# Performance work log

Hardware: AMD Instinct MI355X
Metric: run time of the kernel (lower is better)

The kernel has to match this reference:

```python
import jax, jax.numpy as jnp
import numpy as np

N = 50000       # nodes
E = 800000      # edges
D_IN = 128      # input_dim
HID = 256       # hidden_dim
HEADS = 4
FH = HID // 4   # per-head out dim = 64
OUT = 8         # output_dim
NEG_SLOPE = 0.2 # GATConv leaky_relu slope


def setup_inputs() -> dict:
    key = jax.random.key(0)
    ks = jax.random.split(key, 16)
    def glorot(k, shape):
        fan_in, fan_out = shape[0], shape[-1]
        s = jnp.sqrt(6.0 / (fan_in + fan_out))
        return jax.random.uniform(k, shape, jnp.float32, -s, s)
    inp = {
        "x": jax.random.normal(ks[0], (N, D_IN), jnp.float32),
        "edge_index": jax.random.randint(ks[1], (2, E), 0, N, jnp.int64),
        # GCN layers
        "W1": glorot(ks[2], (D_IN, HID)), "b1": jnp.zeros((HID,), jnp.float32),
        "W2": glorot(ks[3], (HID, HID)), "b2": jnp.zeros((HID,), jnp.float32),
        "W3": glorot(ks[4], (HID, HID // 2)), "b3": jnp.zeros((HID // 2,), jnp.float32),
        # GAT layer: in = HID//2 = 128, out per head = FH, 4 heads concat -> HID
        "Wg": glorot(ks[5], (HID // 2, HEADS * FH)),
        "a_src": glorot(ks[6], (HEADS, FH)),
        "a_dst": glorot(ks[7], (HEADS, FH)),
        "bg": jnp.zeros((HEADS * FH,), jnp.float32),
        # classifier MLP: HID -> HID//2 -> HID//4 -> OUT
        "Wc1": glorot(ks[8], (HID, HID // 2)), "bc1": jnp.zeros((HID // 2,), jnp.float32),
        "Wc2": glorot(ks[9], (HID // 2, HID // 4)), "bc2": jnp.zeros((HID // 4,), jnp.float32),
        "Wc3": glorot(ks[10], (HID // 4, OUT)), "bc3": jnp.zeros((OUT,), jnp.float32),
    }
    return inp


def _with_self_loops(edge_index, n):
    loop = jnp.arange(n, dtype=edge_index.dtype)
    src = jnp.concatenate([edge_index[0], loop])
    dst = jnp.concatenate([edge_index[1], loop])
    return src, dst


def gcn_conv(x, W, b, src, dst, n):
    # PyG GCNConv: h = X W; out = D^{-1/2}(A+I)D^{-1/2} h + b (self loops in src/dst)
    h = x @ W
    deg = jax.ops.segment_sum(jnp.ones_like(dst, jnp.float32), dst, num_segments=n)
    dinv = jnp.where(deg > 0, jax.lax.rsqrt(deg), 0.0)
    norm = dinv[src] * dinv[dst]                      # [E+N]
    out = jax.ops.segment_sum(h[src] * norm[:, None], dst, num_segments=n)
    return out + b


def gat_conv(x, Wg, a_src, a_dst, bg, src, dst, n):
    # PyG GATConv (eval mode, no attn dropout), self loops included in src/dst
    h = (x @ Wg).reshape(n, HEADS, FH)                # [N,H,F]
    al_s = jnp.einsum('nhf,hf->nh', h, a_src)         # [N,H]
    al_d = jnp.einsum('nhf,hf->nh', h, a_dst)
    e = jax.nn.leaky_relu(al_s[src] + al_d[dst], NEG_SLOPE)  # [E+N,H]
    m = jax.ops.segment_max(e, dst, num_segments=n)   # per-dst stable softmax
    ex = jnp.exp(e - m[dst])
    den = jax.ops.segment_sum(ex, dst, num_segments=n)
    alpha = ex / den[dst]                             # [E+N,H]
    out = jax.ops.segment_sum(h[src] * alpha[:, :, None], dst, num_segments=n)
    return out.reshape(n, HEADS * FH) + bg


def reference(x, edge_index, W1, b1, W2, b2, W3, b3, Wg, a_src, a_dst, bg,
              Wc1, bc1, Wc2, bc2, Wc3, bc3):
    n = x.shape[0]
    src, dst = _with_self_loops(edge_index, n)
    h1 = jax.nn.relu(gcn_conv(x, W1, b1, src, dst, n))
    h2 = jax.nn.relu(gcn_conv(h1, W2, b2, src, dst, n)) + h1
    h3 = jax.nn.relu(gcn_conv(h2, W3, b3, src, dst, n))
    h_att = jax.nn.relu(gat_conv(h3, Wg, a_src, a_dst, bg, src, dst, n))
    h_pooled = jnp.mean(h_att, axis=0, keepdims=True)           # [1, HID]
    z = jax.nn.relu(h_pooled @ Wc1 + bc1)
    z = jax.nn.relu(z @ Wc2 + bc2)
    return z @ Wc3 + bc3                                        # [1, OUT]
```

## Files before the change

### kernel.cpp

```cpp
#include <hip/hip_runtime.h>
#include <hip/hip_bf16.h>

#define NNODES 50000
#define NEDGES 800000
#define EN 850000
#define SCAN_B 196

typedef __attribute__((ext_vector_type(8))) short bf16x8;
typedef __attribute__((ext_vector_type(4))) float f32x4;

__device__ __forceinline__ float bf2f(unsigned short u) {
    return __uint_as_float(((unsigned)u) << 16);
}
__device__ __forceinline__ float bflo(unsigned u) { return __uint_as_float(u << 16); }
__device__ __forceinline__ float bfhi(unsigned u) { return __uint_as_float(u & 0xffff0000u); }
__device__ __forceinline__ unsigned short f2bf(float x) {
    unsigned u = __float_as_uint(x);
    u += 0x7fffu + ((u >> 16) & 1u);
    return (unsigned short)(u >> 16);
}
__device__ __forceinline__ unsigned pack2bf(float a, float b) {
    return (unsigned)f2bf(a) | ((unsigned)f2bf(b) << 16);
}
__device__ __forceinline__ void acc8(float* acc, uint4 v, float wg) {
    acc[0] += bflo(v.x) * wg; acc[1] += bfhi(v.x) * wg;
    acc[2] += bflo(v.y) * wg; acc[3] += bfhi(v.y) * wg;
    acc[4] += bflo(v.z) * wg; acc[5] += bfhi(v.z) * wg;
    acc[6] += bflo(v.w) * wg; acc[7] += bfhi(v.w) * wg;
}

__device__ __forceinline__ void split_bf(float x, unsigned short& h, unsigned short& l) {
    unsigned u = __float_as_uint(x);
    h = (unsigned short)(u >> 16);
    float r = x - __uint_as_float(u & 0xffff0000u);
    l = (unsigned short)(__float_as_uint(r) >> 16);
}
__device__ __forceinline__ void do_split(const float* W, unsigned short* Wh, unsigned short* Wl,
                                         int i, int K, int N) {
    int n = i / K, k = i - n * K;
    unsigned short h, l;
    split_bf(W[(size_t)k * N + n], h, l);
    Wh[i] = h; Wl[i] = l;
}

__global__ __launch_bounds__(256) void prep_kernel(const int* __restrict__ ei, float* __restrict__ deg,
                                                   const float* __restrict__ x, unsigned short* __restrict__ xbf,
                                                   const float* __restrict__ W1, const float* __restrict__ W2,
                                                   const float* __restrict__ W3, const float* __restrict__ Wg,
                                                   const float* __restrict__ asr, const float* __restrict__ ads,
                                                   unsigned short* __restrict__ W1th, unsigned short* __restrict__ W1tl,
                                                   unsigned short* __restrict__ W2th, unsigned short* __restrict__ W2tl,
                                                   unsigned short* __restrict__ W3th, unsigned short* __restrict__ W3tl,
                                                   unsigned short* __restrict__ Wgth, unsigned short* __restrict__ Wgtl,
                                                   float* __restrict__ asp, float* __restrict__ adp) {
    int idx = blockIdx.x * 256 + threadIdx.x;
    atomicAdd(&deg[ei[NEDGES + idx]], 1.0f);
    {
        float4 a = *(const float4*)&x[(size_t)idx * 8];
        float4 b = *(const float4*)&x[(size_t)idx * 8 + 4];
        uint4 o;
        o.x = pack2bf(a.x, a.y); o.y = pack2bf(a.z, a.w);
        o.z = pack2bf(b.x, b.y); o.w = pack2bf(b.z, b.w);
        *(uint4*)&xbf[(size_t)idx * 8] = o;
    }
    if (idx < 32768)        do_split(W1, W1th, W1tl, idx, 128, 256);
    else if (idx < 98304)   do_split(W2, W2th, W2tl, idx - 32768, 256, 256);
    else if (idx < 131072)  do_split(W3, W3th, W3tl, idx - 98304, 256, 128);
    else if (idx < 163840)  do_split(Wg, Wgth, Wgtl, idx - 131072, 128, 256);
    else if (idx < 164864) {
        int i0 = idx - 163840;
        int which = i0 >> 9;
        int h = (i0 >> 7) & 3;
        int k = i0 & 127;
        const float* av = (which ? ads : asr) + h * 64;
        const float* wg = Wg + (size_t)k * 256 + h * 64;
        float s = 0.f;
#pragma unroll
        for (int c = 0; c < 64; ++c) s += wg[c] * av[c];
        (which ? adp : asp)[h * 128 + k] = s;
    }
}

__global__ __launch_bounds__(256) void scan_part1(const float* __restrict__ deg, int* __restrict__ row,
                                                  int* __restrict__ bsum, float* __restrict__ dinv) {
    __shared__ int sdata[256];
    int t = threadIdx.x;
    int idx = blockIdx.x * 256 + t;
    float dg = idx < NNODES ? deg[idx] : 0.f;
    if (idx < NNODES) dinv[idx] = rsqrtf(dg + 1.0f);
    int v = idx < NNODES ? (int)dg + 1 : 0;
    sdata[t] = v;
    __syncthreads();
    for (int off = 1; off < 256; off <<= 1) {
        int tmp = t >= off ? sdata[t - off] : 0;
        __syncthreads();
        sdata[t] += tmp;
        __syncthreads();
    }
    if (idx < NNODES) row[idx] = sdata[t] - v;
    if (t == 255) bsum[blockIdx.x] = sdata[255];
}

__global__ __launch_bounds__(256) void scan_part2(int* __restrict__ bsum, int* __restrict__ bofs,
                                                  int* __restrict__ row) {
    __shared__ int sdata[256];
    int t = threadIdx.x;
    int v = t < SCAN_B ? bsum[t] : 0;
    sdata[t] = v;
    __syncthreads();
    for (int off = 1; off < 256; off <<= 1) {
        int tmp = t >= off ? sdata[t - off] : 0;
        __syncthreads();
        sdata[t] += tmp;
        __syncthreads();
    }
    if (t < SCAN_B) bofs[t] = sdata[t] - v;
    if (t == SCAN_B - 1) row[NNODES] = EN - (sdata[t] - v);
}

__global__ __launch_bounds__(256) void scatter_kernel(const int* __restrict__ ei, const int* __restrict__ row,
                                                      const int* __restrict__ bofs,
                                                      int* __restrict__ cursor, const float* __restrict__ dinv,
                                                      uint2* __restrict__ csr) {
    int e = blockIdx.x * blockDim.x + threadIdx.x;
    if (e >= EN) return;
    int s, d;
    if (e < NEDGES) { s = ei[e]; d = ei[NEDGES + e]; } else { s = e - NEDGES; d = s; }
    int pos = row[d] + bofs[d >> 8] + atomicAdd(&cursor[d], 1);
    csr[pos] = make_uint2((unsigned)s, __float_as_uint(dinv[s] * dinv[d]));
}

template<int MODE>
__global__ __launch_bounds__(256) void gemm_bf(const unsigned short* __restrict__ A,
                                               const unsigned short* __restrict__ Wth,
                                               const unsigned short* __restrict__ Wtl,
                                               const float* __restrict__ bias,
                                               unsigned short* __restrict__ C, int M, int K, int Nc) {
    __shared__ unsigned short As[128][40];
    __shared__ unsigned short Bh[128][40], Bl[128][40];
    int t = threadIdx.x;
    int row0 = blockIdx.x * 128, col0 = blockIdx.y * 128;
    int lane = t & 63, w = t >> 6;
    int mb = (w >> 1) * 64, nb = (w & 1) * 64;
    int lr = lane & 15, kg = (lane >> 4) * 8;

    f32x4 acc[4][4];
#pragma unroll
    for (int i = 0; i < 4; ++i)
#pragma unroll
        for (int j = 0; j < 4; ++j) acc[i][j] = (f32x4){0.f, 0.f, 0.f, 0.f};

    for (int k0 = 0; k0 < K; k0 += 32) {
#pragma unroll
        for (int it = 0; it < 2; ++it) {
            int q = it * 256 + t;
            int row = q >> 2, seg = (q & 3) * 8;
            int grow = row0 + row;
            uint4 v = make_uint4(0, 0, 0, 0);
            if (grow < M) v = *(const uint4*)&A[(size_t)grow * K + k0 + seg];
            *(uint4*)&As[row][seg] = v;
        }
#pragma unroll
        for (int it = 0; it < 2; ++it) {
            int o = it * 256 + t;
            int n = o >> 2, ko = (o & 3) * 8;
            size_t g = (size_t)(col0 + n) * K + k0 + ko;
            *(uint4*)&Bh[n][ko] = *(const uint4*)&Wth[g];
            *(uint4*)&Bl[n][ko] = *(const uint4*)&Wtl[g];
        }
        __syncthreads();

        bf16x8 a[4], bh[4], bl[4];
#pragma unroll
        for (int mf = 0; mf < 4; ++mf) a[mf] = *(const bf16x8*)&As[mb + mf * 16 + lr][kg];
#pragma unroll
        for (int nf = 0; nf < 4; ++nf) {
            bh[nf] = *(const bf16x8*)&Bh[nb + nf * 16 + lr][kg];
            bl[nf] = *(const bf16x8*)&Bl[nb + nf * 16 + lr][kg];
        }
#pragma unroll
        for (int mf = 0; mf < 4; ++mf)
#pragma unroll
            for (int nf = 0; nf < 4; ++nf) {
                acc[mf][nf] = __builtin_amdgcn_mfma_f32_16x16x32_bf16(a[mf], bh[nf], acc[mf][nf], 0, 0, 0);
                acc[mf][nf] = __builtin_amdgcn_mfma_f32_16x16x32_bf16(a[mf], bl[nf], acc[mf][nf], 0, 0, 0);
            }
        __syncthreads();
    }

#pragma unroll
    for (int nf = 0; nf < 4; ++nf) {
        int col = col0 + nb + nf * 16 + lr;
        float bv = (MODE == 1) ? bias[col] : 0.f;
#pragma unroll
        for (int mf = 0; mf < 4; ++mf) {
#pragma unroll
            for (int r = 0; r < 4; ++r) {
                int row = row0 + mb + mf * 16 + (lane >> 4) * 4 + r;
                if (row < M) {
                    float v = acc[mf][nf][r];
                    if (MODE == 1) v = fmaxf(v + bv, 0.f);
                    C[(size_t)row * Nc + col] = f2bf(v);
                }
            }
        }
    }
}

template<int NC, int MODE>
__global__ __launch_bounds__(256) void gcn_agg_bf(const unsigned short* __restrict__ h, const int* __restrict__ row,
                                                  const int* __restrict__ bofs, const uint2* __restrict__ csr,
                                                  const float* __restrict__ b, const unsigned short* __restrict__ res,
                                                  const float* __restrict__ asp, const float* __restrict__ adp,
                                                  float* __restrict__ als, float* __restrict__ ald,
                                                  unsigned short* __restrict__ out) {
    int wid = (int)((blockIdx.x * blockDim.x + threadIdx.x) >> 6);
    if (wid >= NNODES) return;
    int lane = threadIdx.x & 63;
    constexpr int LPE = NC / 8;
    constexpr int EPI = 64 / LPE;
    int sub = lane / LPE, li = lane % LPE;
    int col = li * 8;
    float acc[8];
#pragma unroll
    for (int i = 0; i < 8; ++i) acc[i] = 0.f;
    int j0 = row[wid] + bofs[wid >> 8];
    int j1 = row[wid + 1] + bofs[(wid + 1) >> 8];
    int j = j0 + sub;
    for (; j + 3 * EPI < j1; j += 4 * EPI) {
        uint2 c0 = csr[j], c1 = csr[j + EPI], c2 = csr[j + 2 * EPI], c3 = csr[j + 3 * EPI];
        uint4 v0 = *(const uint4*)&h[(size_t)c0.x * NC + col];
        uint4 v1 = *(const uint4*)&h[(size_t)c1.x * NC + col];
        uint4 v2 = *(const uint4*)&h[(size_t)c2.x * NC + col];
        uint4 v3 = *(const uint4*)&h[(size_t)c3.x * NC + col];
        acc8(acc, v0, __uint_as_float(c0.y));
        acc8(acc, v1, __uint_as_float(c1.y));
        acc8(acc, v2, __uint_as_float(c2.y));
        acc8(acc, v3, __uint_as_float(c3.y));
    }
    for (; j < j1; j += EPI) {
        uint2 c0 = csr[j];
        uint4 v0 = *(const uint4*)&h[(size_t)c0.x * NC + col];
        acc8(acc, v0, __uint_as_float(c0.y));
    }
#pragma unroll
    for (int i = 0; i < 8; ++i) {
        acc[i] += __shfl_xor(acc[i], 32);
        if constexpr (EPI == 4) acc[i] += __shfl_xor(acc[i], 16);
    }
    if (lane < LPE) {
        if constexpr (MODE >= 1) {
#pragma unroll
            for (int i = 0; i < 8; ++i) acc[i] = fmaxf(acc[i] + b[col + i], 0.f);
        }
        if constexpr (MODE == 2) {
            uint4 rv = *(const uint4*)&res[(size_t)wid * NC + col];
            acc8(acc, rv, 1.0f);
        }
        uint4 o;
        o.x = pack2bf(acc[0], acc[1]); o.y = pack2bf(acc[2], acc[3]);
        o.z = pack2bf(acc[4], acc[5]); o.w = pack2bf(acc[6], acc[7]);
        *(uint4*)&out[(size_t)wid * NC + col] = o;
        if constexpr (MODE == 3) {
            float s1[4], s2[4];
#pragma unroll
            for (int hh = 0; hh < 4; ++hh) {
                float t1 = 0.f, t2 = 0.f;
#pragma unroll
                for (int i = 0; i < 8; ++i) {
                    t1 += acc[i] * asp[hh * 128 + col + i];
                    t2 += acc[i] * adp[hh * 128 + col + i];
                }
                s1[hh] = t1; s2[hh] = t2;
            }
#pragma unroll
            for (int off = 1; off <= 8; off <<= 1) {
#pragma unroll
                for (int hh = 0; hh < 4; ++hh) {
                    s1[hh] += __shfl_xor(s1[hh], off);
                    s2[hh] += __shfl_xor(s2[hh], off);
                }
            }
            if (lane == 0) {
                *(float4*)&als[wid * 4] = make_float4(s1[0], s1[1], s1[2], s1[3]);
                *(float4*)&ald[wid * 4] = make_float4(s2[0], s2[1], s2[2], s2[3]);
            }
        }
    }
}

__device__ __forceinline__ float lrelu(float x) { return x < 0.f ? 0.2f * x : x; }

__global__ __launch_bounds__(256) void gat_pool(const unsigned short* __restrict__ hg, const int* __restrict__ row,
                                                const int* __restrict__ bofs, const uint2* __restrict__ csr,
                                                const float* __restrict__ als, const float* __restrict__ ald,
                                                const float* __restrict__ bg, float* __restrict__ ppart) {
    __shared__ float alds[4][64][4];
    __shared__ float srows[4][256];
    int wid = (int)((blockIdx.x * blockDim.x + threadIdx.x) >> 6);
    int wv = threadIdx.x >> 6;
    int lane = threadIdx.x & 63;
    int j0 = row[wid] + bofs[wid >> 8];
    int j1 = row[wid + 1] + bofs[(wid + 1) >> 8];
    int deg = j1 - j0;
    float4 ad = *(const float4*)&ald[wid * 4];
    int sub = lane >> 5, li = lane & 31;
    int h = li >> 3;
    int col = li * 8;
    float acc[8];
#pragma unroll
    for (int i = 0; i < 8; ++i) acc[i] = 0.f;

    if (deg <= 64) {
        int sreg = 0;
        float e0 = -1e30f, e1 = -1e30f, e2 = -1e30f, e3 = -1e30f;
        if (lane < deg) {
            sreg = (int)csr[j0 + lane].x;
            float4 as4 = *(const float4*)&als[sreg * 4];
            e0 = lrelu(as4.x + ad.x); e1 = lrelu(as4.y + ad.y);
            e2 = lrelu(as4.z + ad.z); e3 = lrelu(as4.w + ad.w);
        }
        float m0 = e0, m1 = e1, m2 = e2, m3 = e3;
#pragma unroll
        for (int off = 32; off >= 1; off >>= 1) {
            m0 = fmaxf(m0, __shfl_xor(m0, off));
            m1 = fmaxf(m1, __shfl_xor(m1, off));
            m2 = fmaxf(m2, __shfl_xor(m2, off));
            m3 = fmaxf(m3, __shfl_xor(m3, off));
        }
        float x0 = __expf(e0 - m0), x1 = __expf(e1 - m1);
        float x2 = __expf(e2 - m2), x3 = __expf(e3 - m3);
        float d0 = x0, d1 = x1, d2 = x2, d3 = x3;
#pragma unroll
        for (int off = 32; off >= 1; off >>= 1) {
            d0 += __shfl_xor(d0, off);
            d1 += __shfl_xor(d1, off);
            d2 += __shfl_xor(d2, off);
            d3 += __shfl_xor(d3, off);
        }
        *(float4*)&alds[wv][lane][0] = make_float4(x0 / d0, x1 / d1, x2 / d2, x3 / d3);
        int k = sub;
        for (; k + 6 < deg; k += 8) {
            int s0 = __shfl(sreg, k),     s1 = __shfl(sreg, k + 2);
            int s2 = __shfl(sreg, k + 4), s3 = __shfl(sreg, k + 6);
            float a0 = alds[wv][k][h],     a1 = alds[wv][k + 2][h];
            float a2 = alds[wv][k + 4][h], a3 = alds[wv][k + 6][h];
            uint4 v0 = *(const uint4*)&hg[(size_t)s0 * 256 + col];
            uint4 v1 = *(const uint4*)&hg[(size_t)s1 * 256 + col];
            uint4 v2 = *(const uint4*)&hg[(size_t)s2 * 256 + col];
            uint4 v3 = *(const uint4*)&hg[(size_t)s3 * 256 + col];
            acc8(acc, v0, a0); acc8(acc, v1, a1);
            acc8(acc, v2, a2); acc8(acc, v3, a3);
        }
        for (; k < deg; k += 2) {
            int s0 = __shfl(sreg, k);
            float a0 = alds[wv][k][h];
            uint4 v0 = *(const uint4*)&hg[(size_t)s0 * 256 + col];
            acc8(acc, v0, a0);
        }
    } else {
        float m0 = -1e30f, m1 = -1e30f, m2 = -1e30f, m3 = -1e30f;
        float d0 = 0.f, d1 = 0.f, d2 = 0.f, d3 = 0.f;
        for (int j = j0 + lane; j < j1; j += 64) {
            int s = (int)csr[j].x;
            float4 as4 = *(const float4*)&als[s * 4];
            m0 = fmaxf(m0, lrelu(as4.x + ad.x));
            m1 = fmaxf(m1, lrelu(as4.y + ad.y));
            m2 = fmaxf(m2, lrelu(as4.z + ad.z));
            m3 = fmaxf(m3, lrelu(as4.w + ad.w));
        }
#pragma unroll
        for (int off = 32; off >= 1; off >>= 1) {
            m0 = fmaxf(m0, __shfl_xor(m0, off));
            m1 = fmaxf(m1, __shfl_xor(m1, off));
            m2 = fmaxf(m2, __shfl_xor(m2, off));
            m3 = fmaxf(m3, __shfl_xor(m3, off));
        }
        for (int j = j0 + lane; j < j1; j += 64) {
            int s = (int)csr[j].x;
            float4 as4 = *(const float4*)&als[s * 4];
            d0 += __expf(lrelu(as4.x + ad.x) - m0);
            d1 += __expf(lrelu(as4.y + ad.y) - m1);
            d2 += __expf(lrelu(as4.z + ad.z) - m2);
            d3 += __expf(lrelu(as4.w + ad.w) - m3);
        }
#pragma unroll
        for (int off = 32; off >= 1; off >>= 1) {
            d0 += __shfl_xor(d0, off);
            d1 += __shfl_xor(d1, off);
            d2 += __shfl_xor(d2, off);
            d3 += __shfl_xor(d3, off);
        }
        float mh   = h == 0 ? m0 : h == 1 ? m1 : h == 2 ? m2 : m3;
        float invh = 1.f / (h == 0 ? d0 : h == 1 ? d1 : h == 2 ? d2 : d3);
        float adh  = h == 0 ? ad.x : h == 1 ? ad.y : h == 2 ? ad.z : ad.w;
        for (int j = j0 + sub; j < j1; j += 2) {
            uint2 c0 = csr[j];
            float a0 = __expf(lrelu(als[c0.x * 4 + h] + adh) - mh) * invh;
            uint4 v0 = *(const uint4*)&hg[(size_t)c0.x * 256 + col];
            acc8(acc, v0, a0);
        }
    }

#pragma unroll
    for (int i = 0; i < 8; ++i) acc[i] += __shfl_xor(acc[i], 32);
    if (lane < 32) {
#pragma unroll
        for (int i = 0; i < 8; ++i) srows[wv][col + i] = fmaxf(acc[i] + bg[col + i], 0.f);
    }
    __syncthreads();
    int t = threadIdx.x;
    ppart[(size_t)blockIdx.x * 256 + t] = srows[0][t] + srows[1][t] + srows[2][t] + srows[3][t];
}

__global__ __launch_bounds__(256) void reduce_kernel(const float* __restrict__ ppart, float* __restrict__ p2) {
    int t = threadIdx.x;
    int r0 = blockIdx.x * 64;
    int r1 = r0 + 64 < 12500 ? r0 + 64 : 12500;
    float s = 0.f;
    for (int r = r0; r < r1; ++r) s += ppart[(size_t)r * 256 + t];
    p2[blockIdx.x * 256 + t] = s;
}

__global__ __launch_bounds__(256) void mlp_kernel(const float* __restrict__ p2,
                                                  const float* __restrict__ Wc1, const float* __restrict__ bc1,
                                                  const float* __restrict__ Wc2, const float* __restrict__ bc2,
                                                  const float* __restrict__ Wc3, const float* __restrict__ bc3,
                                                  float* __restrict__ out) {
    __shared__ float p[256], z1[128], z2[64];
    int t = threadIdx.x;
    float s0 = 0.f;
    for (int b = 0; b < SCAN_B; ++b) s0 += p2[b * 256 + t];
    p[t] = s0 * (1.0f / NNODES);
    __syncthreads();
    if (t < 128) {
        float s = bc1[t];
        for (int k = 0; k < 256; ++k) s += p[k] * Wc1[k * 128 + t];
        z1[t] = fmaxf(s, 0.f);
    }
    __syncthreads();
    if (t < 64) {
        float s = bc2[t];
        for (int k = 0; k < 128; ++k) s += z1[k] * Wc2[k * 64 + t];
        z2[t] = fmaxf(s, 0.f);
    }
    __syncthreads();
    if (t < 8) {
        float s = bc3[t];
        for (int k = 0; k < 64; ++k) s += z2[k] * Wc3[k * 8 + t];
        out[t] = s;
    }
}

extern "C" void kernel_launch(void* const* d_in, const int* in_sizes, int n_in,
                              void* d_out, int out_size, void* d_ws, size_t ws_size,
                              hipStream_t stream) {
    const float* x   = (const float*)d_in[0];
    const int*   ei  = (const int*)d_in[1];
    const float* W1  = (const float*)d_in[2];  const float* b1  = (const float*)d_in[3];
    const float* W2  = (const float*)d_in[4];  const float* b2  = (const float*)d_in[5];
    const float* W3  = (const float*)d_in[6];  const float* b3  = (const float*)d_in[7];
    const float* Wg  = (const float*)d_in[8];
    const float* asr = (const float*)d_in[9];  const float* ads = (const float*)d_in[10];
    const float* bg  = (const float*)d_in[11];
    const float* Wc1 = (const float*)d_in[12]; const float* bc1 = (const float*)d_in[13];
    const float* Wc2 = (const float*)d_in[14]; const float* bc2 = (const float*)d_in[15];
    const float* Wc3 = (const float*)d_in[16]; const float* bc3 = (const float*)d_in[17];
    float* out = (float*)d_out;

    char* w = (char*)d_ws;
    float* deg    = (float*)w; w += (size_t)NNODES * 4;
    int*   cursor = (int*)w;   w += (size_t)NNODES * 4;
    float* dinv   = (float*)w; w += (size_t)NNODES * 4;
    int*   rowp   = (int*)w;   w += 200016;
    int*   bsum   = (int*)w;   w += 256 * 4;
    int*   bofs   = (int*)w;   w += 256 * 4;
    uint2* csr    = (uint2*)w; w += (size_t)EN * 8;
    float* als    = (float*)w; w += (size_t)NNODES * 4 * 4;
    float* ald    = (float*)w; w += (size_t)NNODES * 4 * 4;
    float* ppart  = (float*)w; w += (size_t)12500 * 256 * 4;
    float* p2     = (float*)w; w += (size_t)SCAN_B * 256 * 4;
    float* asp    = (float*)w; w += 4 * 128 * 4;
    float* adp    = (float*)w; w += 4 * 128 * 4;
    unsigned short* W1th = (unsigned short*)w; w += 128 * 256 * 2;
    unsigned short* W1tl = (unsigned short*)w; w += 128 * 256 * 2;
    unsigned short* W2th = (unsigned short*)w; w += 256 * 256 * 2;
    unsigned short* W2tl = (unsigned short*)w; w += 256 * 256 * 2;
    unsigned short* W3th = (unsigned short*)w; w += 256 * 128 * 2;
    unsigned short* W3tl = (unsigned short*)w; w += 256 * 128 * 2;
    unsigned short* Wgth = (unsigned short*)w; w += 128 * 256 * 2;
    unsigned short* Wgtl = (unsigned short*)w; w += 128 * 256 * 2;
    unsigned short* U1 = (unsigned short*)w; w += (size_t)NNODES * 256 * 2;
    unsigned short* U2 = (unsigned short*)w; w += (size_t)NNODES * 256 * 2;
    unsigned short* U3 = (unsigned short*)w; w += (size_t)NNODES * 256 * 2;
    unsigned short* U4 = (unsigned short*)w; w += (size_t)NNODES * 256 * 2;

    hipMemsetAsync(deg, 0, (size_t)NNODES * 8, stream);
    prep_kernel<<<3125, 256, 0, stream>>>(ei, deg, x, U1, W1, W2, W3, Wg, asr, ads,
                                          W1th, W1tl, W2th, W2tl, W3th, W3tl, Wgth, Wgtl, asp, adp);
    scan_part1<<<SCAN_B, 256, 0, stream>>>(deg, rowp, bsum, dinv);
    scan_part2<<<1, 256, 0, stream>>>(bsum, bofs, rowp);
    scatter_kernel<<<(EN + 255) / 256, 256, 0, stream>>>(ei, rowp, bofs, cursor, dinv, csr);

    dim3 gA((NNODES + 127) / 128, 2);
    dim3 gB((NNODES + 127) / 128, 1);
    int aggBlocks = (NNODES * 64 + 255) / 256;

    gcn_agg_bf<128, 0><<<aggBlocks, 256, 0, stream>>>(U1, rowp, bofs, csr, nullptr, nullptr,
                                                      nullptr, nullptr, nullptr, nullptr, U2);
    gemm_bf<1><<<gA, 256, 0, stream>>>(U2, W1th, W1tl, b1, U3, NNODES, 128, 256);

    gemm_bf<0><<<gA, 256, 0, stream>>>(U3, W2th, W2tl, nullptr, U1, NNODES, 256, 256);
    gcn_agg_bf<256, 2><<<aggBlocks, 256, 0, stream>>>(U1, rowp, bofs, csr, b2, U3,
                                                      nullptr, nullptr, nullptr, nullptr, U2);

    gemm_bf<0><<<gB, 256, 0, stream>>>(U2, W3th, W3tl, nullptr, U4, NNODES, 256, 128);
    gcn_agg_bf<128, 3><<<aggBlocks, 256, 0, stream>>>(U4, rowp, bofs, csr, b3, nullptr,
                                                      asp, adp, als, ald, U1);

    gemm_bf<0><<<gA, 256, 0, stream>>>(U1, Wgth, Wgtl, nullptr, U2, NNODES, 128, 256);
    gat_pool<<<aggBlocks, 256, 0, stream>>>(U2, rowp, bofs, csr, als, ald, bg, ppart);

    reduce_kernel<<<SCAN_B, 256, 0, stream>>>(ppart, p2);
    mlp_kernel<<<1, 256, 0, stream>>>(p2, Wc1, bc1, Wc2, bc2, Wc3, bc3, out);
}
```

Before: 496.7 us.

## Fuse CSR-building prologue into one cooperative kernel with grid syncs

Replaces the memset, prep, two scan kernels and scatter kernel with a single cooperative kernel that uses grid-wide syncs between phases, keeping the old launches as a fallback if the cooperative launch fails. This is meant to remove several kernel launch gaps and the separate memset. In exchange the work runs on a fixed grid of 512 blocks with grid-stride loops, and each grid sync carries its own cost. A variable in the GAT aggregation loop is also renamed.

```diff
diff --git a/kernel.cpp b/kernel.cpp
--- a/kernel.cpp
+++ b/kernel.cpp
@@ -1,10 +1,14 @@
 #include <hip/hip_runtime.h>
 #include <hip/hip_bf16.h>
+#include <hip/hip_cooperative_groups.h>
+
+namespace cg = cooperative_groups;
 
 #define NNODES 50000
 #define NEDGES 800000
 #define EN 850000
 #define SCAN_B 196
+#define COOP_B 512
 
 typedef __attribute__((ext_vector_type(8))) short bf16x8;
 typedef __attribute__((ext_vector_type(4))) float f32x4;
@@ -41,6 +45,113 @@
     unsigned short h, l;
     split_bf(W[(size_t)k * N + n], h, l);
     Wh[i] = h; Wl[i] = l;
+}
+
+__device__ __forceinline__ void prep_item(int i, const int* ei, float* deg, const float* x,
+                                          unsigned short* xbf,
+                                          const float* W1, const float* W2, const float* W3, const float* Wg,
+                                          const float* asr, const float* ads,
+                                          unsigned short* W1th, unsigned short* W1tl,
+                                          unsigned short* W2th, unsigned short* W2tl,
+                                          unsigned short* W3th, unsigned short* W3tl,
+                                          unsigned short* Wgth, unsigned short* Wgtl,
+                                          float* asp, float* adp) {
+    atomicAdd(&deg[ei[NEDGES + i]], 1.0f);
+    {
+        float4 a = *(const float4*)&x[(size_t)i * 8];
+        float4 b = *(const float4*)&x[(size_t)i * 8 + 4];
+        uint4 o;
+        o.x = pack2bf(a.x, a.y); o.y = pack2bf(a.z, a.w);
+        o.z = pack2bf(b.x, b.y); o.w = pack2bf(b.z, b.w);
+        *(uint4*)&xbf[(size_t)i * 8] = o;
+    }
+    if (i < 32768)        do_split(W1, W1th, W1tl, i, 128, 256);
+    else if (i < 98304)   do_split(W2, W2th, W2tl, i - 32768, 256, 256);
+    else if (i < 131072)  do_split(W3, W3th, W3tl, i - 98304, 256, 128);
+    else if (i < 163840)  do_split(Wg, Wgth, Wgtl, i - 131072, 128, 256);
+    else if (i < 164864) {
+        int i0 = i - 163840;
+        int which = i0 >> 9, hh = (i0 >> 7) & 3, k = i0 & 127;
+        const float* av = (which ? ads : asr) + hh * 64;
+        const float* wg = Wg + (size_t)k * 256 + hh * 64;
+        float s = 0.f;
+#pragma unroll
+        for (int c = 0; c < 64; ++c) s += wg[c] * av[c];
+        (which ? adp : asp)[hh * 128 + k] = s;
+    }
+}
+
+__global__ __launch_bounds__(256, 2) void coop_prologue(
+    const int* __restrict__ ei, const float* __restrict__ x,
+    const float* __restrict__ W1, const float* __restrict__ W2,
+    const float* __restrict__ W3, const float* __restrict__ Wg,
+    const float* __restrict__ asr, const float* __restrict__ ads,
+    float* __restrict__ deg, int* __restrict__ cursor, float* __restrict__ dinv,
+    int* __restrict__ rowp, int* __restrict__ bsum, int* __restrict__ bofs,
+    uint2* __restrict__ csr, unsigned short* __restrict__ xbf,
+    unsigned short* __restrict__ W1th, unsigned short* __restrict__ W1tl,
+    unsigned short* __restrict__ W2th, unsigned short* __restrict__ W2tl,
+    unsigned short* __restrict__ W3th, unsigned short* __restrict__ W3tl,
+    unsigned short* __restrict__ Wgth, unsigned short* __restrict__ Wgtl,
+    float* __restrict__ asp, float* __restrict__ adp) {
+    __shared__ int sdata[256];
+    cg::grid_group grid = cg::this_grid();
+    int t = threadIdx.x;
+    int tid = blockIdx.x * 256 + t;
+    int nthr = gridDim.x * 256;
+
+    for (int i = tid; i < NNODES; i += nthr) { deg[i] = 0.f; cursor[i] = 0; }
+    __threadfence();
+    grid.sync();
+
+    for (int i = tid; i < NEDGES; i += nthr)
+        prep_item(i, ei, deg, x, xbf, W1, W2, W3, Wg, asr, ads,
+                  W1th, W1tl, W2th, W2tl, W3th, W3tl, Wgth, Wgtl, asp, adp);
+    __threadfence();
+    grid.sync();
+
+    for (int c = blockIdx.x; c < SCAN_B; c += gridDim.x) {
+        int idx = c * 256 + t;
+        float dg = idx < NNODES ? deg[idx] : 0.f;
+        if (idx < NNODES) dinv[idx] = rsqrtf(dg + 1.0f);
+        int v = idx < NNODES ? (int)dg + 1 : 0;
+        sdata[t] = v;
+        __syncthreads();
+        for (int off = 1; off < 256; off <<= 1) {
+            int tmp = t >= off ? sdata[t - off] : 0;
+            __syncthreads();
+            sdata[t] += tmp;
+            __syncthreads();
+        }
+        if (idx < NNODES) rowp[idx] = sdata[t] - v;
+        if (t == 255) bsum[c] = sdata[255];
+        __syncthreads();
+    }
+    __threadfence();
+    grid.sync();
+
+    if (blockIdx.x == 0) {
+        int v = t < SCAN_B ? bsum[t] : 0;
+        sdata[t] = v;
+        __syncthreads();
+        for (int off = 1; off < 256; off <<= 1) {
+            int tmp = t >= off ? sdata[t - off] : 0;
+            __syncthreads();
+            sdata[t] += tmp;
+            __syncthreads();
+        }
+        if (t < SCAN_B) bofs[t] = sdata[t] - v;
+        if (t == SCAN_B - 1) rowp[NNODES] = EN - (sdata[t] - v);
+    }
+    __threadfence();
+    grid.sync();
+
+    for (int e = tid; e < EN; e += nthr) {
+        int s, d;
+        if (e < NEDGES) { s = ei[e]; d = ei[NEDGES + e]; } else { s = e - NEDGES; d = s; }
+        int pos = rowp[d] + bofs[d >> 8] + atomicAdd(&cursor[d], 1);
+        csr[pos] = make_uint2((unsigned)s, __float_as_uint(dinv[s] * dinv[d]));
+    }
 }
 
 __global__ __launch_bounds__(256) void prep_kernel(const int* __restrict__ ei, float* __restrict__ deg,
@@ -54,31 +165,8 @@
                                                    unsigned short* __restrict__ Wgth, unsigned short* __restrict__ Wgtl,
                                                    float* __restrict__ asp, float* __restrict__ adp) {
     int idx = blockIdx.x * 256 + threadIdx.x;
-    atomicAdd(&deg[ei[NEDGES + idx]], 1.0f);
-    {
-        float4 a = *(const float4*)&x[(size_t)idx * 8];
-        float4 b = *(const float4*)&x[(size_t)idx * 8 + 4];
-        uint4 o;
-        o.x = pack2bf(a.x, a.y); o.y = pack2bf(a.z, a.w);
-        o.z = pack2bf(b.x, b.y); o.w = pack2bf(b.z, b.w);
-        *(uint4*)&xbf[(size_t)idx * 8] = o;
-    }
-    if (idx < 32768)        do_split(W1, W1th, W1tl, idx, 128, 256);
-    else if (idx < 98304)   do_split(W2, W2th, W2tl, idx - 32768, 256, 256);
-    else if (idx < 131072)  do_split(W3, W3th, W3tl, idx - 98304, 256, 128);
-    else if (idx < 163840)  do_split(Wg, Wgth, Wgtl, idx - 131072, 128, 256);
-    else if (idx < 164864) {
-        int i0 = idx - 163840;
-        int which = i0 >> 9;
-        int h = (i0 >> 7) & 3;
-        int k = i0 & 127;
-        const float* av = (which ? ads : asr) + h * 64;
-        const float* wg = Wg + (size_t)k * 256 + h * 64;
-        float s = 0.f;
-#pragma unroll
-        for (int c = 0; c < 64; ++c) s += wg[c] * av[c];
-        (which ? adp : asp)[h * 128 + k] = s;
-    }
+    prep_item(idx, ei, deg, x, xbf, W1, W2, W3, Wg, asr, ads,
+              W1th, W1tl, W2th, W2tl, W3th, W3tl, Wgth, Wgtl, asp, adp);
 }
 
 __global__ __launch_bounds__(256) void scan_part1(const float* __restrict__ deg, int* __restrict__ row,
@@ -341,12 +429,12 @@
         *(float4*)&alds[wv][lane][0] = make_float4(x0 / d0, x1 / d1, x2 / d2, x3 / d3);
         int k = sub;
         for (; k + 6 < deg; k += 8) {
-            int s0 = __shfl(sreg, k),     s1 = __shfl(sreg, k + 2);
+            int s0 = __shfl(sreg, k),     int1 = __shfl(sreg, k + 2);
             int s2 = __shfl(sreg, k + 4), s3 = __shfl(sreg, k + 6);
             float a0 = alds[wv][k][h],     a1 = alds[wv][k + 2][h];
             float a2 = alds[wv][k + 4][h], a3 = alds[wv][k + 6][h];
             uint4 v0 = *(const uint4*)&hg[(size_t)s0 * 256 + col];
-            uint4 v1 = *(const uint4*)&hg[(size_t)s1 * 256 + col];
+            uint4 v1 = *(const uint4*)&hg[(size_t)int1 * 256 + col];
             uint4 v2 = *(const uint4*)&hg[(size_t)s2 * 256 + col];
             uint4 v3 = *(const uint4*)&hg[(size_t)s3 * 256 + col];
             acc8(acc, v0, a0); acc8(acc, v1, a1);
@@ -495,12 +583,23 @@
     unsigned short* U3 = (unsigned short*)w; w += (size_t)NNODES * 256 * 2;
     unsigned short* U4 = (unsigned short*)w; w += (size_t)NNODES * 256 * 2;
 
-    hipMemsetAsync(deg, 0, (size_t)NNODES * 8, stream);
-    prep_kernel<<<3125, 256, 0, stream>>>(ei, deg, x, U1, W1, W2, W3, Wg, asr, ads,
-                                          W1th, W1tl, W2th, W2tl, W3th, W3tl, Wgth, Wgtl, asp, adp);
-    scan_part1<<<SCAN_B, 256, 0, stream>>>(deg, rowp, bsum, dinv);
-    scan_part2<<<1, 256, 0, stream>>>(bsum, bofs, rowp);
-    scatter_kernel<<<(EN + 255) / 256, 256, 0, stream>>>(ei, rowp, bofs, cursor, dinv, csr);
+    void* cargs[] = {(void*)&ei, (void*)&x, (void*)&W1, (void*)&W2, (void*)&W3, (void*)&Wg,
+                     (void*)&asr, (void*)&ads,
+                     (void*)&deg, (void*)&cursor, (void*)&dinv, (void*)&rowp, (void*)&bsum, (void*)&bofs,
+                     (void*)&csr, (void*)&U1,
+                     (void*)&W1th, (void*)&W1tl, (void*)&W2th, (void*)&W2tl,
+                     (void*)&W3th, (void*)&W3tl, (void*)&Wgth, (void*)&Wgtl,
+                     (void*)&asp, (void*)&adp};
+    hipError_t cerr = hipLaunchCooperativeKernel((const void*)coop_prologue, dim3(COOP_B), dim3(256),
+                                                 cargs, 0, stream);
+    if (cerr != hipSuccess) {
+        hipMemsetAsync(deg, 0, (size_t)NNODES * 8, stream);
+        prep_kernel<<<3125, 256, 0, stream>>>(ei, deg, x, U1, W1, W2, W3, Wg, asr, ads,
+                                              W1th, W1tl, W2th, W2tl, W3th, W3tl, Wgth, Wgtl, asp, adp);
+        scan_part1<<<SCAN_B, 256, 0, stream>>>(deg, rowp, bsum, dinv);
+        scan_part2<<<1, 256, 0, stream>>>(bsum, bofs, rowp);
+        scatter_kernel<<<(EN + 255) / 256, 256, 0, stream>>>(ei, rowp, bofs, cursor, dinv, csr);
+    }
 
     dim3 gA((NNODES + 127) / 128, 2);
     dim3 gB((NNODES + 127) / 128, 1);
```

After: 847.9 us. 70.7% more time.
